# Kernel tuning notes

Measured on AMD Instinct MI355X. Metric: run time of the kernel, lower is better.

Reference implementation:

```python
import jax, jax.numpy as jnp
import numpy as np

NEG = -9e15
ALPHA = 0.2  # leaky-relu slope


def gat_layer(h, mask, W, a, concat):
    # h: [N, Fin], W: [Fin, Fout], a: [2*Fout, 1], mask: [N, N]
    Wh = h @ W                                   # [N, Fout]
    F = Wh.shape[1]
    e = jax.nn.leaky_relu(Wh @ a[:F] + (Wh @ a[F:]).T, ALPHA)  # [N, N]
    att = jax.nn.softmax(jnp.where(mask > 0, e, NEG), axis=1)
    out = att @ Wh                               # [N, Fout]
    return jax.nn.elu(out) if concat else out


def gat(x, mask, W, a, Wo, ao):
    # W: [H, Fin, Fhid], a: [H, 2*Fhid, 1]
    heads = jax.vmap(lambda Wi, ai: gat_layer(x, mask, Wi, ai, True))(W, a)  # [H, N, Fhid]
    h = jnp.transpose(heads, (1, 0, 2)).reshape(x.shape[0], -1)  # [N, H*Fhid] (concat dim=1)
    return jax.nn.elu(gat_layer(h, mask, Wo, ao, False))


def setup_inputs() -> dict:
    key = jax.random.key(0)
    ks = jax.random.split(key, 16)
    N, Fin, H, Fhid, Ffin, P = 4096, 256, 4, 64, 64, 16
    x = jax.random.normal(ks[0], (N, Fin), jnp.float32)
    eye = jnp.eye(N, dtype=jnp.float32)
    sadj = jnp.maximum((jax.random.uniform(ks[1], (N, N)) < 0.005).astype(jnp.float32), eye)
    sadj2 = jnp.maximum((jax.random.uniform(ks[2], (N, N)) < 0.005).astype(jnp.float32), eye)
    s = 0.1
    inp = {
        "x": x, "sadj": sadj, "sadj2": sadj2,
        "W1": s * jax.random.normal(ks[3], (H, Fin, Fhid), jnp.float32),
        "a1": s * jax.random.normal(ks[4], (H, 2 * Fhid, 1), jnp.float32),
        "Wo1": s * jax.random.normal(ks[5], (H * Fhid, Ffin), jnp.float32),
        "ao1": s * jax.random.normal(ks[6], (2 * Ffin, 1), jnp.float32),
        "W2": s * jax.random.normal(ks[7], (H, Fin, Fhid), jnp.float32),
        "a2": s * jax.random.normal(ks[8], (H, 2 * Fhid, 1), jnp.float32),
        "Wo2": s * jax.random.normal(ks[9], (H * Fhid, Ffin), jnp.float32),
        "ao2": s * jax.random.normal(ks[10], (2 * Ffin, 1), jnp.float32),
        "Wp1": s * jax.random.normal(ks[11], (Ffin, P), jnp.float32),
        "bp1": jnp.zeros((P,), jnp.float32),
        "Wp2": s * jax.random.normal(ks[12], (P, 1), jnp.float32),
    }
    return inp


def reference(x, sadj, sadj2, W1, a1, Wo1, ao1, W2, a2, Wo2, ao2, Wp1, bp1, Wp2):
    emb1 = gat(x, sadj, W1, a1, Wo1, ao1)    # [N, Ffin]
    emb2 = gat(x, sadj2, W2, a2, Wo2, ao2)   # [N, Ffin]
    emb = jnp.stack([emb1, emb2], axis=1)    # [N, 2, Ffin]
    w = jnp.tanh(emb @ Wp1 + bp1) @ Wp2      # [N, 2, 1]
    beta = jax.nn.softmax(w, axis=1)
    return jnp.sum(beta * emb, axis=1)       # [N, Ffin]
```

## Files before the change

### kernel.cpp

```cpp
#include <hip/hip_runtime.h>
#include <hip/hip_bf16.h>
#include <stdint.h>


typedef short short8 __attribute__((ext_vector_type(8)));
typedef __bf16 bf16x8 __attribute__((ext_vector_type(8)));
typedef float floatx4 __attribute__((ext_vector_type(4)));

#define MAXDEG 128
#define LRELU 0.2f

template <typename V>
__device__ inline auto mfma_impl(V a, V b, floatx4 c, int)
    -> decltype(__builtin_amdgcn_mfma_f32_16x16x32_bf16(a, b, c, 0, 0, 0)) {
  return __builtin_amdgcn_mfma_f32_16x16x32_bf16(a, b, c, 0, 0, 0);
}
template <typename V>
__device__ inline floatx4 mfma_impl(V a, V b, floatx4 c, long) {
  return __builtin_amdgcn_mfma_f32_16x16x32_bf16(
      __builtin_bit_cast(bf16x8, a), __builtin_bit_cast(bf16x8, b), c, 0, 0, 0);
}
__device__ inline floatx4 MFMA16(short8 a, short8 b, floatx4 c) {
  return mfma_impl(a, b, c, 0);
}

__device__ inline bool is_bf16_inputs(const void* sadj) {
  return ((*(const uint32_t*)sadj) & 0xFFFFu) == 0x3F80u;
}
__device__ inline float ldval(const void* p, size_t i, bool isbf) {
  if (isbf) return __bfloat162float(((const __hip_bfloat16*)p)[i]);
  return ((const float*)p)[i];
}
__device__ inline uint16_t f2bf_bits(float f) {
  __hip_bfloat16 h = __float2bfloat16(f);
  return *(uint16_t*)&h;
}

static constexpr size_t OFF_ADJ = 0;
static constexpr size_t OFF_DEG = OFF_ADJ + (size_t)2 * 4096 * MAXDEG * 4;
static constexpr size_t OFF_XB  = OFF_DEG + (size_t)2 * 4096 * 4;
static constexpr size_t OFF_WT  = OFF_XB  + (size_t)4096 * 256 * 2;
static constexpr size_t OFF_WOT = OFF_WT  + (size_t)2 * 4 * 64 * 256 * 2;
static constexpr size_t OFF_AV  = OFF_WOT + (size_t)2 * 64 * 256 * 2;
static constexpr size_t OFF_AOV = OFF_AV  + (size_t)2 * 4 * 128 * 4;
static constexpr size_t OFF_WP1 = OFF_AOV + (size_t)2 * 128 * 4;
static constexpr size_t OFF_BP1 = OFF_WP1 + (size_t)64 * 16 * 4;
static constexpr size_t OFF_WP2 = OFF_BP1 + 64;
static constexpr size_t OFF_WH1 = OFF_WP2 + 192;
static constexpr size_t OFF_S1  = OFF_WH1 + (size_t)2 * 4096 * 256 * 4;
static constexpr size_t OFF_D1  = OFF_S1  + (size_t)2 * 4 * 4096 * 4;
static constexpr size_t OFF_H2  = OFF_D1  + (size_t)2 * 4 * 4096 * 4;
static constexpr size_t OFF_WH2 = OFF_H2  + (size_t)2 * 4096 * 256 * 2;
static constexpr size_t OFF_S2  = OFF_WH2 + (size_t)2 * 4096 * 64 * 4;
static constexpr size_t OFF_D2  = OFF_S2  + (size_t)2 * 4096 * 4;
static constexpr size_t OFF_EMB = OFF_D2  + (size_t)2 * 4096 * 4;

__global__ __launch_bounds__(256) void k_conv(const void* x,
    const void* W1, const void* W2, const void* Wo1, const void* Wo2,
    const void* a1, const void* a2, const void* ao1, const void* ao2,
    const void* wp1, const void* bp1, const void* wp2, const void* sadj,
    uint16_t* xb, uint16_t* Wt, uint16_t* Wot,
    float* Av, float* Aov, float* Wp1v, float* Bp1v, float* Wp2v) {
  bool isbf = is_bf16_inputs(sadj);
  int bid = blockIdx.x;
  if (bid < 1024) {
    int i0 = (bid * 256 + threadIdx.x) * 4;
    if (isbf) {
      *(uint64_t*)(xb + i0) = *(const uint64_t*)((const uint16_t*)x + i0);
    } else {
      const float* xf = (const float*)x;
      float4 f = *(const float4*)(xf + i0);
      xb[i0 + 0] = f2bf_bits(f.x);
      xb[i0 + 1] = f2bf_bits(f.y);
      xb[i0 + 2] = f2bf_bits(f.z);
      xb[i0 + 3] = f2bf_bits(f.w);
    }
    return;
  }
  int idx = (bid - 1024) * 256 + threadIdx.x;
  if (idx < 131072) {
    int k = idx & 255, f = (idx >> 8) & 63, h = (idx >> 14) & 3, g = idx >> 16;
    const void* W = g ? W2 : W1;
    Wt[idx] = f2bf_bits(ldval(W, (size_t)h * 16384 + (size_t)k * 64 + f, isbf));
  } else if (idx < 163840) {
    int j = idx - 131072;
    int k = j & 255, f = (j >> 8) & 63, g = j >> 14;
    const void* W = g ? Wo2 : Wo1;
    Wot[j] = f2bf_bits(ldval(W, (size_t)k * 64 + f, isbf));
  } else if (idx < 166176) {
    int q = idx - 163840;
    if (q < 512)        Av[q] = ldval(a1, q, isbf);
    else if (q < 1024)  Av[q] = ldval(a2, q - 512, isbf);
    else if (q < 1152)  Aov[q - 1024] = ldval(ao1, q - 1024, isbf);
    else if (q < 1280)  Aov[q - 1152 + 128] = ldval(ao2, q - 1152, isbf);
    else if (q < 2304)  Wp1v[q - 1280] = ldval(wp1, q - 1280, isbf);
    else if (q < 2320)  Bp1v[q - 2304] = ldval(bp1, q - 2304, isbf);
    else                Wp2v[q - 2320] = ldval(wp2, q - 2320, isbf);
  }
}

__global__ __launch_bounds__(256) void k_adj(const void* sadj, const void* sadj2,
                                             int* adj, int* deg) {
  int w = blockIdx.x * 4 + (threadIdx.x >> 6);
  int lane = threadIdx.x & 63;
  int g = w >> 12, n = w & 4095;
  bool isbf = is_bf16_inputs(sadj);
  const void* mask = g ? sadj2 : sadj;
  int* out = adj + (size_t)w * MAXDEG;
  uint64_t bits = 0;
  if (isbf) {
    const uint16_t* mrow = (const uint16_t*)mask + (size_t)n * 4096;
    uint4 v[8];
#pragma unroll
    for (int t = 0; t < 8; ++t) v[t] = *(const uint4*)(mrow + t * 512 + lane * 8);
#pragma unroll
    for (int t = 0; t < 8; ++t) {
      uint32_t wd[4] = {v[t].x, v[t].y, v[t].z, v[t].w};
#pragma unroll
      for (int k = 0; k < 8; ++k) {
        uint16_t val = (uint16_t)(wd[k >> 1] >> ((k & 1) * 16));
        if (val != 0 && !(val & 0x8000)) bits |= 1ull << (t * 8 + k);
      }
    }
  } else {
    const float* mrow = (const float*)mask + (size_t)n * 4096;
    float4 v[16];
#pragma unroll
    for (int t = 0; t < 16; ++t) v[t] = *(const float4*)(mrow + t * 256 + lane * 4);
#pragma unroll
    for (int t = 0; t < 16; ++t) {
      float vals[4] = {v[t].x, v[t].y, v[t].z, v[t].w};
#pragma unroll
      for (int k = 0; k < 4; ++k)
        if (vals[k] > 0.f) bits |= 1ull << (t * 4 + k);
    }
  }
  int c = __popcll(bits);
  int pre = c;
#pragma unroll
  for (int o = 1; o < 64; o <<= 1) {
    int tv = __shfl_up(pre, o);
    if (lane >= o) pre += tv;
  }
  int total = __shfl(pre, 63);
  int off = pre - c;
  while (bits) {
    int i = __ffsll((unsigned long long)bits) - 1;
    bits &= bits - 1;
    int col = isbf ? ((i >> 3) * 512 + lane * 8 + (i & 7))
                   : ((i >> 2) * 256 + lane * 4 + (i & 3));
    if (off < MAXDEG) out[off] = col;
    ++off;
  }
  if (lane == 0) deg[w] = total < MAXDEG ? total : MAXDEG;
}

__global__ __launch_bounds__(256) void k_gemm1(const uint16_t* xb, const uint16_t* Wt,
                                               const float* Av,
                                               float* Wh1, float* s1, float* d1) {
  int w = blockIdx.x * 4 + (threadIdx.x >> 6);
  int lane = threadIdx.x & 63;
  int q = lane >> 4, c = lane & 15;
  int g = w >> 10, rem = w & 1023;
  int m0 = (rem >> 2) << 4, h = rem & 3;
  const uint16_t* B = Wt + (size_t)(g * 4 + h) * 64 * 256;
  floatx4 acc[4] = {};
  const uint16_t* arow = xb + (size_t)(m0 + c) * 256 + q * 8;
  for (int kk = 0; kk < 8; ++kk) {
    short8 a = *(const short8*)(arow + kk * 32);
#pragma unroll
    for (int t = 0; t < 4; ++t) {
      short8 b = *(const short8*)(B + (size_t)(t * 16 + c) * 256 + kk * 32 + q * 8);
      acc[t] = MFMA16(a, b, acc[t]);
    }
  }
  float* Crow = Wh1 + (size_t)(g * 4096 + m0) * 256 + h * 64;
#pragma unroll
  for (int t = 0; t < 4; ++t)
#pragma unroll
    for (int r = 0; r < 4; ++r)
      Crow[(size_t)(q * 4 + r) * 256 + t * 16 + c] = acc[t][r];
  const float* ag = Av + (g * 4 + h) * 128;
  float as[4], ad[4];
#pragma unroll
  for (int t = 0; t < 4; ++t) { as[t] = ag[t * 16 + c]; ad[t] = ag[64 + t * 16 + c]; }
#pragma unroll
  for (int r = 0; r < 4; ++r) {
    float ps = 0.f, pd = 0.f;
#pragma unroll
    for (int t = 0; t < 4; ++t) { ps += acc[t][r] * as[t]; pd += acc[t][r] * ad[t]; }
#pragma unroll
    for (int o = 1; o < 16; o <<= 1) { ps += __shfl_xor(ps, o); pd += __shfl_xor(pd, o); }
    if (c == 0) {
      int n = m0 + q * 4 + r;
      s1[((size_t)(g * 4096 + n)) * 4 + h] = ps;
      d1[((size_t)(g * 4096 + n)) * 4 + h] = pd;
    }
  }
}

__global__ __launch_bounds__(256) void k_gemm2(const uint16_t* h2, const uint16_t* Wot,
                                               const float* Aov,
                                               float* Wh2, float* s2, float* d2) {
  int w = blockIdx.x * 4 + (threadIdx.x >> 6);
  int lane = threadIdx.x & 63;
  int q = lane >> 4, c = lane & 15;
  int g = w >> 8, m0 = (w & 255) << 4;
  const uint16_t* A = h2 + (size_t)g * 4096 * 256;
  const uint16_t* B = Wot + (size_t)g * 64 * 256;
  floatx4 acc[4] = {};
  const uint16_t* arow = A + (size_t)(m0 + c) * 256 + q * 8;
  for (int kk = 0; kk < 8; ++kk) {
    short8 a = *(const short8*)(arow + kk * 32);
#pragma unroll
    for (int t = 0; t < 4; ++t) {
      short8 b = *(const short8*)(B + (size_t)(t * 16 + c) * 256 + kk * 32 + q * 8);
      acc[t] = MFMA16(a, b, acc[t]);
    }
  }
  float* Crow = Wh2 + (size_t)(g * 4096 + m0) * 64;
#pragma unroll
  for (int t = 0; t < 4; ++t)
#pragma unroll
    for (int r = 0; r < 4; ++r)
      Crow[(size_t)(q * 4 + r) * 64 + t * 16 + c] = acc[t][r];
  const float* ag = Aov + g * 128;
  float as[4], ad[4];
#pragma unroll
  for (int t = 0; t < 4; ++t) { as[t] = ag[t * 16 + c]; ad[t] = ag[64 + t * 16 + c]; }
#pragma unroll
  for (int r = 0; r < 4; ++r) {
    float ps = 0.f, pd = 0.f;
#pragma unroll
    for (int t = 0; t < 4; ++t) { ps += acc[t][r] * as[t]; pd += acc[t][r] * ad[t]; }
#pragma unroll
    for (int o = 1; o < 16; o <<= 1) { ps += __shfl_xor(ps, o); pd += __shfl_xor(pd, o); }
    if (c == 0) {
      int n = m0 + q * 4 + r;
      s2[g * 4096 + n] = ps;
      d2[g * 4096 + n] = pd;
    }
  }
}

__global__ __launch_bounds__(256) void k_att1(const int* adj, const int* deg,
    const float* s1, const float* d1, const float* Wh1, uint16_t* h2) {
  __shared__ float pbuf[4][4][MAXDEG];
  __shared__ int jbuf[4][MAXDEG];
  int wv = threadIdx.x >> 6, lane = threadIdx.x & 63;
  int w = blockIdx.x * 4 + wv;
  int g = w >> 12;
  int gn = w;
  int dg = deg[gn];
  const int* nbr = adj + (size_t)gn * MAXDEG;
  float4 s4 = *(const float4*)(s1 + (size_t)gn * 4);
  const float4* d4 = (const float4*)(d1) + (size_t)g * 4096;

  bool v0 = lane < dg, v1 = lane + 64 < dg;
  int j0 = 0, j1 = 0;
  if (v0) j0 = nbr[lane];
  if (v1) j1 = nbr[lane + 64];
  float4 dj0 = d4[j0];
  float4 dj1 = d4[j1];
  if (v0) jbuf[wv][lane] = j0;
  if (v1) jbuf[wv][lane + 64] = j1;

  const float ninf = -3.0e38f;
  float sa[4] = {s4.x, s4.y, s4.z, s4.w};
  float d0a[4] = {dj0.x, dj0.y, dj0.z, dj0.w};
  float d1a[4] = {dj1.x, dj1.y, dj1.z, dj1.w};
#pragma unroll
  for (int h = 0; h < 4; ++h) {
    float t0 = sa[h] + d0a[h]; t0 = t0 > 0.f ? t0 : LRELU * t0;
    float t1 = sa[h] + d1a[h]; t1 = t1 > 0.f ? t1 : LRELU * t1;
    float e0 = v0 ? t0 : ninf;
    float e1 = v1 ? t1 : ninf;
    float m = fmaxf(e0, e1);
#pragma unroll
    for (int o = 32; o; o >>= 1) m = fmaxf(m, __shfl_xor(m, o));
    float p0 = v0 ? __expf(e0 - m) : 0.f;
    float p1 = v1 ? __expf(e1 - m) : 0.f;
    float l = p0 + p1;
#pragma unroll
    for (int o = 32; o; o >>= 1) l += __shfl_xor(l, o);
    float inv = __frcp_rn(l);
    pbuf[wv][h][lane] = p0 * inv;
    pbuf[wv][h][lane + 64] = p1 * inv;
  }
  int myh = lane >> 4;
  const float* prow = pbuf[wv][myh];
  const int* jb = jbuf[wv];
  const float4* Wg = (const float4*)(Wh1) + (size_t)g * 4096 * 64;
  float ax = 0.f, ay = 0.f, az = 0.f, aw = 0.f;
  int i = 0;
  for (; i + 4 <= dg; i += 4) {
    int ja = jb[i], jb2 = jb[i + 1], jc = jb[i + 2], jd = jb[i + 3];
    float pa = prow[i], pb = prow[i + 1], pc = prow[i + 2], pd = prow[i + 3];
    float4 wa = Wg[(size_t)ja * 64 + lane];
    float4 wb = Wg[(size_t)jb2 * 64 + lane];
    float4 wc = Wg[(size_t)jc * 64 + lane];
    float4 wd = Wg[(size_t)jd * 64 + lane];
    ax += pa * wa.x + pb * wb.x + pc * wc.x + pd * wd.x;
    ay += pa * wa.y + pb * wb.y + pc * wc.y + pd * wd.y;
    az += pa * wa.z + pb * wb.z + pc * wc.z + pd * wd.z;
    aw += pa * wa.w + pb * wb.w + pc * wc.w + pd * wd.w;
  }
  for (; i < dg; ++i) {
    int j = jb[i];
    float p = prow[i];
    float4 wa = Wg[(size_t)j * 64 + lane];
    ax += p * wa.x; ay += p * wa.y; az += p * wa.z; aw += p * wa.w;
  }
  ax = ax > 0.f ? ax : __expf(ax) - 1.f;
  ay = ay > 0.f ? ay : __expf(ay) - 1.f;
  az = az > 0.f ? az : __expf(az) - 1.f;
  aw = aw > 0.f ? aw : __expf(aw) - 1.f;
  ushort4 o4 = {f2bf_bits(ax), f2bf_bits(ay), f2bf_bits(az), f2bf_bits(aw)};
  *(ushort4*)(h2 + (size_t)gn * 256 + lane * 4) = o4;
}

__global__ __launch_bounds__(256) void k_att2(const int* adj, const int* deg,
    const float* s2, const float* d2, const float* Wh2, float* emb) {
  __shared__ float pbuf[4][MAXDEG];
  __shared__ int jbuf[4][MAXDEG];
  int wv = threadIdx.x >> 6, lane = threadIdx.x & 63;
  int w = blockIdx.x * 4 + wv;
  int g = w >> 12;
  int gn = w;
  int dg = deg[gn];
  const int* nbr = adj + (size_t)gn * MAXDEG;
  float sn = s2[gn];
  const float* dp = d2 + (size_t)g * 4096;

  bool v0 = lane < dg, v1 = lane + 64 < dg;
  int j0 = 0, j1 = 0;
  if (v0) j0 = nbr[lane];
  if (v1) j1 = nbr[lane + 64];
  float dd0 = dp[j0], dd1 = dp[j1];
  if (v0) jbuf[wv][lane] = j0;
  if (v1) jbuf[wv][lane + 64] = j1;

  const float ninf = -3.0e38f;
  float t0 = sn + dd0; t0 = t0 > 0.f ? t0 : LRELU * t0;
  float t1 = sn + dd1; t1 = t1 > 0.f ? t1 : LRELU * t1;
  float e0 = v0 ? t0 : ninf;
  float e1 = v1 ? t1 : ninf;
  float m = fmaxf(e0, e1);
#pragma unroll
  for (int o = 32; o; o >>= 1) m = fmaxf(m, __shfl_xor(m, o));
  float p0 = v0 ? __expf(e0 - m) : 0.f;
  float p1 = v1 ? __expf(e1 - m) : 0.f;
  float l = p0 + p1;
#pragma unroll
  for (int o = 32; o; o >>= 1) l += __shfl_xor(l, o);
  float inv = __frcp_rn(l);
  pbuf[wv][lane] = p0 * inv;
  pbuf[wv][lane + 64] = p1 * inv;

  int mye = lane >> 4, c4 = lane & 15;
  const float4* Wg = (const float4*)(Wh2) + (size_t)g * 4096 * 16;
  float ax = 0.f, ay = 0.f, az = 0.f, aw = 0.f;
  for (int i = 0; i < dg; i += 4) {
    int idx = i + mye;
    bool vv = idx < dg;
    int sidx = vv ? idx : 0;
    int j = jbuf[wv][sidx];
    float p = vv ? pbuf[wv][sidx] : 0.f;
    float4 wa = Wg[(size_t)j * 16 + c4];
    ax += p * wa.x; ay += p * wa.y; az += p * wa.z; aw += p * wa.w;
  }
#pragma unroll
  for (int o = 16; o <= 32; o <<= 1) {
    ax += __shfl_xor(ax, o);
    ay += __shfl_xor(ay, o);
    az += __shfl_xor(az, o);
    aw += __shfl_xor(aw, o);
  }
  if (lane < 16) {
    ax = ax > 0.f ? ax : __expf(ax) - 1.f;
    ay = ay > 0.f ? ay : __expf(ay) - 1.f;
    az = az > 0.f ? az : __expf(az) - 1.f;
    aw = aw > 0.f ? aw : __expf(aw) - 1.f;
    float4 r = {ax, ay, az, aw};
    *(float4*)(emb + (size_t)gn * 64 + lane * 4) = r;
  }
}

__global__ __launch_bounds__(256) void k_final(const float* emb, const float* Wp1v,
    const float* Bp1v, const float* Wp2v, const void* sadj, void* out) {
  __shared__ float se[4][128];
  __shared__ float st[4][32];
  __shared__ float sw[4][2];
  int wv = threadIdx.x >> 6, lane = threadIdx.x & 63;
  int n = blockIdx.x * 4 + wv;
  bool isbf = is_bf16_inputs(sadj);
  float e1 = emb[(size_t)n * 64 + lane];
  float e2 = emb[(size_t)(4096 + n) * 64 + lane];
  se[wv][lane] = e1;
  se[wv][64 + lane] = e2;
  __syncthreads();
  if (lane < 32) {
    int g = lane >> 4, p = lane & 15;
    float s = Bp1v[p];
    const float* eb = &se[wv][g * 64];
    for (int f = 0; f < 64; ++f) s += eb[f] * Wp1v[f * 16 + p];
    st[wv][lane] = tanhf(s);
  }
  __syncthreads();
  if (lane < 2) {
    float s = 0.f;
    for (int p = 0; p < 16; ++p) s += st[wv][lane * 16 + p] * Wp2v[p];
    sw[wv][lane] = s;
  }
  __syncthreads();
  float w0 = sw[wv][0], w1 = sw[wv][1];
  float mx = fmaxf(w0, w1);
  float p0 = __expf(w0 - mx), p1 = __expf(w1 - mx);
  float inv = 1.f / (p0 + p1);
  float v = (p0 * e1 + p1 * e2) * inv;
  if (isbf) ((uint16_t*)out)[(size_t)n * 64 + lane] = f2bf_bits(v);
  else ((float*)out)[(size_t)n * 64 + lane] = v;
}

extern "C" void kernel_launch(void* const* d_in, const int* in_sizes, int n_in,
                              void* d_out, int out_size, void* d_ws, size_t ws_size,
                              hipStream_t stream) {
  const void* x    = d_in[0];
  const void* sadj = d_in[1];
  const void* sadj2 = d_in[2];
  const void* W1  = d_in[3];
  const void* a1  = d_in[4];
  const void* Wo1 = d_in[5];
  const void* ao1 = d_in[6];
  const void* W2  = d_in[7];
  const void* a2  = d_in[8];
  const void* Wo2 = d_in[9];
  const void* ao2 = d_in[10];
  const void* Wp1 = d_in[11];
  const void* bp1 = d_in[12];
  const void* Wp2 = d_in[13];

  char* ws = (char*)d_ws;
  int* adj      = (int*)(ws + OFF_ADJ);
  int* deg      = (int*)(ws + OFF_DEG);
  uint16_t* xb  = (uint16_t*)(ws + OFF_XB);
  uint16_t* Wt  = (uint16_t*)(ws + OFF_WT);
  uint16_t* Wot = (uint16_t*)(ws + OFF_WOT);
  float* Av     = (float*)(ws + OFF_AV);
  float* Aov    = (float*)(ws + OFF_AOV);
  float* Wp1v   = (float*)(ws + OFF_WP1);
  float* Bp1v   = (float*)(ws + OFF_BP1);
  float* Wp2v   = (float*)(ws + OFF_WP2);
  float* Wh1    = (float*)(ws + OFF_WH1);
  float* s1     = (float*)(ws + OFF_S1);
  float* d1     = (float*)(ws + OFF_D1);
  uint16_t* h2  = (uint16_t*)(ws + OFF_H2);
  float* Wh2    = (float*)(ws + OFF_WH2);
  float* s2     = (float*)(ws + OFF_S2);
  float* d2     = (float*)(ws + OFF_D2);
  float* emb    = (float*)(ws + OFF_EMB);

  k_conv<<<1680, 256, 0, stream>>>(x, W1, W2, Wo1, Wo2, a1, a2, ao1, ao2,
                                   Wp1, bp1, Wp2, sadj,
                                   xb, Wt, Wot, Av, Aov, Wp1v, Bp1v, Wp2v);
  k_adj<<<2048, 256, 0, stream>>>(sadj, sadj2, adj, deg);
  k_gemm1<<<512, 256, 0, stream>>>(xb, Wt, Av, Wh1, s1, d1);
  k_att1<<<2048, 256, 0, stream>>>(adj, deg, s1, d1, Wh1, h2);
  k_gemm2<<<128, 256, 0, stream>>>(h2, Wot, Aov, Wh2, s2, d2);
  k_att2<<<2048, 256, 0, stream>>>(adj, deg, s2, d2, Wh2, emb);
  k_final<<<1024, 256, 0, stream>>>(emb, Wp1v, Bp1v, Wp2v, sadj, d_out);
}
```

Measured before the change: 229.5 us.

## Split mask scan into streaming bitmask pass and compaction; unroll neighbor gathers

Replaces the per-row adjacency kernel with two kernels. The first is a grid-stride streaming scan that reads both masks with nontemporal loads and writes a packed bitmask. The second is a compaction kernel that builds neighbor lists from that bitmask. It also unrolls the gather loops in both attention kernels so more Wh loads are in flight at once. The aim is better memory throughput on the dominant 128MB mask read, at the cost of an extra launch and an intermediate bitmask buffer.

```diff
diff --git a/kernel.cpp b/kernel.cpp
--- a/kernel.cpp
+++ b/kernel.cpp
@@ -6,6 +6,7 @@
 typedef short short8 __attribute__((ext_vector_type(8)));
 typedef __bf16 bf16x8 __attribute__((ext_vector_type(8)));
 typedef float floatx4 __attribute__((ext_vector_type(4)));
+typedef unsigned int uintx4 __attribute__((ext_vector_type(4)));
 
 #define MAXDEG 128
 #define LRELU 0.2f
@@ -54,6 +55,7 @@
 static constexpr size_t OFF_S2  = OFF_WH2 + (size_t)2 * 4096 * 64 * 4;
 static constexpr size_t OFF_D2  = OFF_S2  + (size_t)2 * 4096 * 4;
 static constexpr size_t OFF_EMB = OFF_D2  + (size_t)2 * 4096 * 4;
+static constexpr size_t OFF_MB  = OFF_EMB + (size_t)2 * 4096 * 64 * 4;
 
 __global__ __launch_bounds__(256) void k_conv(const void* x,
     const void* W1, const void* W2, const void* Wo1, const void* Wo2,
@@ -99,42 +101,52 @@
   }
 }
 
-__global__ __launch_bounds__(256) void k_adj(const void* sadj, const void* sadj2,
-                                             int* adj, int* deg) {
+__global__ __launch_bounds__(256) void k_scan(const void* sadj, const void* sadj2,
+                                              uint8_t* mbytes) {
+  bool isbf = is_bf16_inputs(sadj);
+  int tid = blockIdx.x * blockDim.x + threadIdx.x;
+  int nt = gridDim.x * blockDim.x;
+  const int NCHUNK = 4194304;
+  if (isbf) {
+    const uint16_t* m0 = (const uint16_t*)sadj;
+    const uint16_t* m1 = (const uint16_t*)sadj2;
+    for (int c = tid; c < NCHUNK; c += nt) {
+      const uint16_t* src = (c < 2097152) ? m0 : m1;
+      int cc = c & 2097151;
+      uintx4 v = __builtin_nontemporal_load((const uintx4*)src + cc);
+      uint32_t wd[4] = {v.x, v.y, v.z, v.w};
+      uint32_t byte = 0;
+#pragma unroll
+      for (int k = 0; k < 8; ++k) {
+        uint16_t val = (uint16_t)(wd[k >> 1] >> ((k & 1) * 16));
+        if (val != 0 && !(val & 0x8000)) byte |= 1u << k;
+      }
+      mbytes[c] = (uint8_t)byte;
+    }
+  } else {
+    const float* m0 = (const float*)sadj;
+    const float* m1 = (const float*)sadj2;
+    for (int c = tid; c < NCHUNK; c += nt) {
+      const float* src = (c < 2097152) ? m0 : m1;
+      size_t cc = (size_t)(c & 2097151) * 8;
+      floatx4 va = __builtin_nontemporal_load((const floatx4*)(src + cc));
+      floatx4 vb = __builtin_nontemporal_load((const floatx4*)(src + cc + 4));
+      float vals[8] = {va.x, va.y, va.z, va.w, vb.x, vb.y, vb.z, vb.w};
+      uint32_t byte = 0;
+#pragma unroll
+      for (int k = 0; k < 8; ++k)
+        if (vals[k] > 0.f) byte |= 1u << k;
+      mbytes[c] = (uint8_t)byte;
+    }
+  }
+}
+
+__global__ __launch_bounds__(256) void k_compact(const uint8_t* mbytes,
+                                                 int* adj, int* deg) {
   int w = blockIdx.x * 4 + (threadIdx.x >> 6);
   int lane = threadIdx.x & 63;
-  int g = w >> 12, n = w & 4095;
-  bool isbf = is_bf16_inputs(sadj);
-  const void* mask = g ? sadj2 : sadj;
+  uint64_t bits = *((const uint64_t*)(mbytes + (size_t)w * 512) + lane);
   int* out = adj + (size_t)w * MAXDEG;
-  uint64_t bits = 0;
-  if (isbf) {
-    const uint16_t* mrow = (const uint16_t*)mask + (size_t)n * 4096;
-    uint4 v[8];
-#pragma unroll
-    for (int t = 0; t < 8; ++t) v[t] = *(const uint4*)(mrow + t * 512 + lane * 8);
-#pragma unroll
-    for (int t = 0; t < 8; ++t) {
-      uint32_t wd[4] = {v[t].x, v[t].y, v[t].z, v[t].w};
-#pragma unroll
-      for (int k = 0; k < 8; ++k) {
-        uint16_t val = (uint16_t)(wd[k >> 1] >> ((k & 1) * 16));
-        if (val != 0 && !(val & 0x8000)) bits |= 1ull << (t * 8 + k);
-      }
-    }
-  } else {
-    const float* mrow = (const float*)mask + (size_t)n * 4096;
-    float4 v[16];
-#pragma unroll
-    for (int t = 0; t < 16; ++t) v[t] = *(const float4*)(mrow + t * 256 + lane * 4);
-#pragma unroll
-    for (int t = 0; t < 16; ++t) {
-      float vals[4] = {v[t].x, v[t].y, v[t].z, v[t].w};
-#pragma unroll
-      for (int k = 0; k < 4; ++k)
-        if (vals[k] > 0.f) bits |= 1ull << (t * 4 + k);
-    }
-  }
   int c = __popcll(bits);
   int pre = c;
 #pragma unroll
@@ -144,12 +156,11 @@
   }
   int total = __shfl(pre, 63);
   int off = pre - c;
+  int base = lane * 64;
   while (bits) {
     int i = __ffsll((unsigned long long)bits) - 1;
     bits &= bits - 1;
-    int col = isbf ? ((i >> 3) * 512 + lane * 8 + (i & 7))
-                   : ((i >> 2) * 256 + lane * 4 + (i & 3));
-    if (off < MAXDEG) out[off] = col;
+    if (off < MAXDEG) out[off] = base + i;
     ++off;
   }
   if (lane == 0) deg[w] = total < MAXDEG ? total : MAXDEG;
@@ -292,24 +303,25 @@
   const int* jb = jbuf[wv];
   const float4* Wg = (const float4*)(Wh1) + (size_t)g * 4096 * 64;
   float ax = 0.f, ay = 0.f, az = 0.f, aw = 0.f;
-  int i = 0;
-  for (; i + 4 <= dg; i += 4) {
-    int ja = jb[i], jb2 = jb[i + 1], jc = jb[i + 2], jd = jb[i + 3];
-    float pa = prow[i], pb = prow[i + 1], pc = prow[i + 2], pd = prow[i + 3];
-    float4 wa = Wg[(size_t)ja * 64 + lane];
-    float4 wb = Wg[(size_t)jb2 * 64 + lane];
-    float4 wc = Wg[(size_t)jc * 64 + lane];
-    float4 wd = Wg[(size_t)jd * 64 + lane];
-    ax += pa * wa.x + pb * wb.x + pc * wc.x + pd * wd.x;
-    ay += pa * wa.y + pb * wb.y + pc * wc.y + pd * wd.y;
-    az += pa * wa.z + pb * wb.z + pc * wc.z + pd * wd.z;
-    aw += pa * wa.w + pb * wb.w + pc * wc.w + pd * wd.w;
-  }
-  for (; i < dg; ++i) {
-    int j = jb[i];
-    float p = prow[i];
-    float4 wa = Wg[(size_t)j * 64 + lane];
-    ax += p * wa.x; ay += p * wa.y; az += p * wa.z; aw += p * wa.w;
+  for (int i = 0; i < dg; i += 8) {
+    float pv[8];
+    float4 wv8[8];
+#pragma unroll
+    for (int k = 0; k < 8; ++k) {
+      int idx = i + k;
+      bool vv = idx < dg;
+      int sidx = vv ? idx : 0;
+      int j = jb[sidx];
+      pv[k] = vv ? prow[sidx] : 0.f;
+      wv8[k] = Wg[(size_t)j * 64 + lane];
+    }
+#pragma unroll
+    for (int k = 0; k < 8; ++k) {
+      ax += pv[k] * wv8[k].x;
+      ay += pv[k] * wv8[k].y;
+      az += pv[k] * wv8[k].z;
+      aw += pv[k] * wv8[k].w;
+    }
   }
   ax = ax > 0.f ? ax : __expf(ax) - 1.f;
   ay = ay > 0.f ? ay : __expf(ay) - 1.f;
@@ -360,14 +372,19 @@
   int mye = lane >> 4, c4 = lane & 15;
   const float4* Wg = (const float4*)(Wh2) + (size_t)g * 4096 * 16;
   float ax = 0.f, ay = 0.f, az = 0.f, aw = 0.f;
-  for (int i = 0; i < dg; i += 4) {
-    int idx = i + mye;
-    bool vv = idx < dg;
-    int sidx = vv ? idx : 0;
-    int j = jbuf[wv][sidx];
-    float p = vv ? pbuf[wv][sidx] : 0.f;
-    float4 wa = Wg[(size_t)j * 16 + c4];
-    ax += p * wa.x; ay += p * wa.y; az += p * wa.z; aw += p * wa.w;
+  for (int i = 0; i < dg; i += 8) {
+    int ia = i + mye, ib = i + 4 + mye;
+    bool va = ia < dg, vb = ib < dg;
+    int sa_ = va ? ia : 0, sb_ = vb ? ib : 0;
+    int ja = jbuf[wv][sa_], jb2 = jbuf[wv][sb_];
+    float pa = va ? pbuf[wv][sa_] : 0.f;
+    float pb = vb ? pbuf[wv][sb_] : 0.f;
+    float4 wa = Wg[(size_t)ja * 16 + c4];
+    float4 wb = Wg[(size_t)jb2 * 16 + c4];
+    ax += pa * wa.x + pb * wb.x;
+    ay += pa * wa.y + pb * wb.y;
+    az += pa * wa.z + pb * wb.z;
+    aw += pa * wa.w + pb * wb.w;
   }
 #pragma unroll
   for (int o = 16; o <= 32; o <<= 1) {
@@ -459,11 +476,13 @@
   float* s2     = (float*)(ws + OFF_S2);
   float* d2     = (float*)(ws + OFF_D2);
   float* emb    = (float*)(ws + OFF_EMB);
-
+  uint8_t* mb   = (uint8_t*)(ws + OFF_MB);
+
+  k_scan<<<1024, 256, 0, stream>>>(sadj, sadj2, mb);
   k_conv<<<1680, 256, 0, stream>>>(x, W1, W2, Wo1, Wo2, a1, a2, ao1, ao2,
                                    Wp1, bp1, Wp2, sadj,
                                    xb, Wt, Wot, Av, Aov, Wp1v, Bp1v, Wp2v);
-  k_adj<<<2048, 256, 0, stream>>>(sadj, sadj2, adj, deg);
+  k_compact<<<2048, 256, 0, stream>>>(mb, adj, deg);
   k_gemm1<<<512, 256, 0, stream>>>(xb, Wt, Av, Wh1, s1, d1);
   k_att1<<<2048, 256, 0, stream>>>(adj, deg, s1, d1, Wh1, h2);
   k_gemm2<<<128, 256, 0, stream>>>(h2, Wot, Aov, Wh2, s2, d2);
```

After: 225.1 us. Within noise of the previous version (-1.9%).
